# Performance work log

Measured on AMD Instinct MI355X. Metric: run time of the kernel, lower is better.

Reference implementation:

```python
import jax, jax.numpy as jnp
import numpy as np

ALPHA1 = 0.5
ALPHA2 = 0.5
EXP_WEIGHTED = False
N = 16384


def setup_inputs() -> dict:
    key = jax.random.key(0)
    k1, k2 = jax.random.split(key)
    inp = jax.random.normal(k1, (N,), dtype=jnp.float32)
    tgt = jax.random.uniform(k2, (N,), dtype=jnp.float32)
    return {"input": inp, "target": tgt}


def reference(input, target):
    n = input.shape[0]
    # mask[i, j] = target[j] > target[i]  (pairs where j is ranked above i)
    mask = target[None, :] > target[:, None]  # [N, N] bool
    # BPR term: log(1 + exp(-(input[j] - input[i]))) == softplus(input[i] - input[j])
    bpr = jax.nn.softplus(input[:, None] - input[None, :])  # [N, N]
    # MSE term depends only on row i, broadcast over j
    mse = (input - target) ** 2  # [N]
    x = ALPHA1 * bpr + ALPHA2 * mse[:, None]  # [N, N]
    if EXP_WEIGHTED:
        w = jnp.expm1(target)  # exp(target) - 1
        x = w[:, None] * w[None, :] * x
    # x[x < 0] = 0, and only masked pairs contribute
    x = jnp.where(mask, jnp.maximum(x, 0.0), 0.0)
    total = jnp.sum(x)
    if EXP_WEIGHTED:
        scale = 2.0 / (n * (jnp.e - 1.0)) ** 2
    else:
        scale = 2.0 / n ** 2
    return scale * total
```

## Files before the change

### kernel.cpp

```cpp
#include <hip/hip_runtime.h>


#define N_ELEM 16384
#define NBUCK  4096
#define CHUNK  256
#define NPAIR  511
#define NBLK   512
#define PF     0xAAAAAAAAu

__device__ __forceinline__ float fexp2(float x){ return __builtin_amdgcn_exp2f(x); }
__device__ __forceinline__ float flog2(float x){ return __builtin_amdgcn_logf(x); }

__global__ __launch_bounds__(1024, 8) void fused_kernel(
    const float* __restrict__ input, const float* __restrict__ target,
    float* __restrict__ wsA, int* __restrict__ cntA, int* __restrict__ gdone,
    float* __restrict__ out)
{
    const float L2E   = 1.4426950408889634f;
    const float INVN2 = 1.0f / (16384.0f * 16384.0f);
    const int b = blockIdx.x, tid = threadIdx.x, lane = tid & 63;
    const int wu = __builtin_amdgcn_readfirstlane((int)(threadIdx.x >> 6));

    __shared__ int histLds[NBUCK];
    __shared__ __align__(16) float cLds[CHUNK];
    __shared__ float wsLds[16];
    __shared__ int   wtot[16];

    float vsum = 0.0f;

    if (b == NPAIR) {
        for (int q = tid; q < NBUCK; q += 1024) histLds[q] = 0;
        __syncthreads();
        int packed[16];
        #pragma unroll
        for (int q = 0; q < 16; ++q) {
            const int idx = (q << 10) + tid;
            const float t = target[idx];
            int bk = (int)(t * 4096.0f);
            bk = bk < 0 ? 0 : (bk > 4095 ? 4095 : bk);
            const int ticket = atomicAdd(&histLds[bk], 1);
            packed[q] = (bk << 15) | ticket;
        }
        __syncthreads();
        int v[4], le[4]; int s = 0;
        #pragma unroll
        for (int q = 0; q < 4; ++q) v[q] = histLds[4 * tid + q];
        #pragma unroll
        for (int q = 0; q < 4; ++q) { le[q] = s; s += v[q]; }
        int inc = s;
        #pragma unroll
        for (int d = 1; d < 64; d <<= 1) {
            int n = __shfl_up(inc, d, 64); if (lane >= d) inc += n;
        }
        if (lane == 63) wtot[wu] = inc;
        __syncthreads();
        int woff = 0;
        #pragma unroll
        for (int w = 0; w < 16; ++w) woff += (w < wu) ? wtot[w] : 0;
        const int texcl = woff + (inc - s);
        #pragma unroll
        for (int q = 0; q < 4; ++q) histLds[4 * tid + q] = texcl + le[q];
        __syncthreads();
        #pragma unroll
        for (int q = 0; q < 16; ++q) {
            const int idx = (q << 10) + tid;
            const int pos = histLds[packed[q] >> 15] + (packed[q] & 0x7FFF);
            const float x = input[idx], t = target[idx];
            const float d = x - t;
            vsum += (-x * (float)pos + d * d * (float)(16383 - pos)) * INVN2;
        }
    } else {
        const int ntb = (b < 475) ? 4 : 5;
        const int u0  = (b < 475) ? (b << 2) : (1900 + 5 * (b - 475));
        int cj = (int)((sqrtf(8.0f * (float)u0 + 1.0f) - 1.0f) * 0.5f);
        while ((cj + 1) * (cj + 2) / 2 <= u0) ++cj;
        while (cj * (cj + 1) / 2 > u0) --cj;
        int ci = u0 - cj * (cj + 1) / 2;

        float la0 = 0.0f, la1 = 0.0f;
        int   cnt = 0;
        int   cjCur = -1;
        for (int m = 0; m < ntb; ++m) {
            if (cj != cjCur) {
                __syncthreads();
                if (tid < CHUNK)
                    cLds[tid] = 0.5f * fexp2(input[cj * CHUNK + tid] * L2E);
                cjCur = cj;
                __syncthreads();
            }
            float Xh[4];
            #pragma unroll
            for (int k = 0; k < 4; ++k)
                Xh[k] = 0.5f * fexp2(input[ci * CHUNK + 64 * k + lane] * L2E);
            const float4* __restrict__ cp4 = (const float4*)(cLds + wu * 16);
            const float4 A = cp4[0], B = cp4[1], C = cp4[2], D = cp4[3];

            if (ci != cj) {
                #pragma unroll
                for (int k = 0; k < 4; ++k) {
                    const float X = Xh[k];
                    float p = (X + A.x) * (X + A.y);
                    p *= (X + A.z) * (X + A.w);
                    p *= (X + B.x) * (X + B.y);
                    p *= (X + B.z) * (X + B.w);
                    p *= (X + C.x) * (X + C.y);
                    p *= (X + C.z) * (X + C.w);
                    p *= (X + D.x) * (X + D.y);
                    p *= (X + D.z) * (X + D.w);
                    if (k & 1) la1 += flog2(p); else la0 += flog2(p);
                }
                cnt += 64;
            } else {
                const int jb = wu * 16;
                #pragma unroll
                for (int k = 0; k < 4; ++k) {
                    const float X = Xh[k];
                    const int rr = 64 * k + lane;
                    float p = 1.0f; int c = 0;
                    #define PRD(col, q) do { const bool ok = (jb + (q)) > rr;   \
                        p *= ok ? (X + (col)) : 1.0f; c += ok ? 1 : 0; } while (0)
                    PRD(A.x,0);  PRD(A.y,1);  PRD(A.z,2);  PRD(A.w,3);
                    PRD(B.x,4);  PRD(B.y,5);  PRD(B.z,6);  PRD(B.w,7);
                    PRD(C.x,8);  PRD(C.y,9);  PRD(C.z,10); PRD(C.w,11);
                    PRD(D.x,12); PRD(D.y,13); PRD(D.z,14); PRD(D.w,15);
                    #undef PRD
                    if (k & 1) la1 += flog2(p); else la0 += flog2(p);
                    cnt += c;
                }
            }
            if (ci == cj) { ++cj; ci = 0; } else { ++ci; }
        }
        vsum = (la0 + la1 + (float)cnt) * (0.6931471805599453f * INVN2);
    }

    #pragma unroll
    for (int off = 32; off; off >>= 1) vsum += __shfl_down(vsum, off, 64);
    if (lane == 0) wsLds[wu] = vsum;
    __syncthreads();

    if (wu == 0) {
        float s = (lane < 16) ? wsLds[lane] : 0.0f;
        #pragma unroll
        for (int off = 8; off; off >>= 1) s += __shfl_down(s, off, 64);
        int isFinal = 0;
        if (lane == 0) {
            const int g = b & 63;
            float* slot  = wsA  + 32 * g;
            int*   cslot = cntA + 32 * g;
            const float old = __hip_atomic_fetch_add(slot, s,
                __ATOMIC_RELAXED, __HIP_MEMORY_SCOPE_AGENT);
            asm volatile("s_waitcnt vmcnt(0)" :: "v"(old) : "memory");
            const unsigned tkt = (unsigned)__hip_atomic_fetch_add(cslot, 1,
                __ATOMIC_RELAXED, __HIP_MEMORY_SCOPE_AGENT) - PF;
            if (tkt == 7u) {
                asm volatile("s_waitcnt vmcnt(0)" ::: "memory");
                const unsigned gd = (unsigned)__hip_atomic_fetch_add(gdone, 1,
                    __ATOMIC_RELAXED, __HIP_MEMORY_SCOPE_AGENT) - PF;
                isFinal = (gd == 63u);
            }
        }
        isFinal = __shfl(isFinal, 0, 64);
        if (isFinal) {
            float v = __hip_atomic_fetch_add(wsA + 32 * lane, 0.0f,
                __ATOMIC_RELAXED, __HIP_MEMORY_SCOPE_AGENT);
            #pragma unroll
            for (int off = 32; off; off >>= 1) v += __shfl_down(v, off, 64);
            if (lane == 0)
                out[0] = v - 64.0f * __uint_as_float(PF);
        }
    }
}

extern "C" void kernel_launch(void* const* d_in, const int* in_sizes, int n_in,
                              void* d_out, int out_size, void* d_ws, size_t ws_size,
                              hipStream_t stream) {
    const float* input  = (const float*)d_in[0];
    const float* target = (const float*)d_in[1];
    float* out   = (float*)d_out;
    int*   wsi   = (int*)d_ws;
    int*   gdone = wsi + 8;
    float* wsA   = (float*)d_ws + 32768;
    int*   cntA  = wsi + 65536;

    fused_kernel<<<NBLK, 1024, 0, stream>>>(input, target, wsA, cntA, gdone, out);
}
```

Before: 73.04 us.

## Symmetrize diagonal tiles and halve grid with more tiles per block

Diagonal tiles now compute the full unmasked product over all 256x256 pairs and take half, using the symmetry softplus(a-b)+softplus(b-a) = (a-b) + 2*softplus(b-a). The linear half-term and a ln2/2 offset per element move into the histogram block's per-element term. This removes the per-element masking and select work in diagonal tiles. The grid shrinks from 512 to 256 blocks, each handling 8 or 9 tiles, and the exp scaling is folded into an fma. Fewer blocks lowers launch and reduction overhead but gives less parallelism and a longer serial histogram block relative to the others.

```diff
diff --git a/kernel.cpp b/kernel.cpp
--- a/kernel.cpp
+++ b/kernel.cpp
@@ -4,14 +4,14 @@
 #define N_ELEM 16384
 #define NBUCK  4096
 #define CHUNK  256
-#define NPAIR  511
-#define NBLK   512
+#define NPAIR  255
+#define NBLK   256
 #define PF     0xAAAAAAAAu
 
 __device__ __forceinline__ float fexp2(float x){ return __builtin_amdgcn_exp2f(x); }
 __device__ __forceinline__ float flog2(float x){ return __builtin_amdgcn_logf(x); }
 
-__global__ __launch_bounds__(1024, 8) void fused_kernel(
+__global__ __launch_bounds__(1024) void fused_kernel(
     const float* __restrict__ input, const float* __restrict__ target,
     float* __restrict__ wsA, int* __restrict__ cntA, int* __restrict__ gdone,
     float* __restrict__ out)
@@ -67,70 +67,66 @@
             const int pos = histLds[packed[q] >> 15] + (packed[q] & 0x7FFF);
             const float x = input[idx], t = target[idx];
             const float d = x - t;
-            vsum += (-x * (float)pos + d * d * (float)(16383 - pos)) * INVN2;
+            vsum += (-x * ((float)pos + 0.5f)
+                     + d * d * (float)(16383 - pos)
+                     - 0.34657359027997264f) * INVN2;
         }
     } else {
-        const int ntb = (b < 475) ? 4 : 5;
-        const int u0  = (b < 475) ? (b << 2) : (1900 + 5 * (b - 475));
+        const int ntb = (b < 215) ? 8 : 9;
+        const int u0  = (b < 215) ? (b << 3) : (1720 + 9 * (b - 215));
         int cj = (int)((sqrtf(8.0f * (float)u0 + 1.0f) - 1.0f) * 0.5f);
         while ((cj + 1) * (cj + 2) / 2 <= u0) ++cj;
         while (cj * (cj + 1) / 2 > u0) --cj;
         int ci = u0 - cj * (cj + 1) / 2;
 
         float la0 = 0.0f, la1 = 0.0f;
-        int   cnt = 0;
+        float laD = 0.0f;
+        int   ntD = 0;
         int   cjCur = -1;
         for (int m = 0; m < ntb; ++m) {
             if (cj != cjCur) {
                 __syncthreads();
                 if (tid < CHUNK)
-                    cLds[tid] = 0.5f * fexp2(input[cj * CHUNK + tid] * L2E);
+                    cLds[tid] = fexp2(fmaf(input[cj * CHUNK + tid], L2E, -1.0f));
                 cjCur = cj;
                 __syncthreads();
             }
             float Xh[4];
             #pragma unroll
             for (int k = 0; k < 4; ++k)
-                Xh[k] = 0.5f * fexp2(input[ci * CHUNK + 64 * k + lane] * L2E);
+                Xh[k] = fexp2(fmaf(input[ci * CHUNK + 64 * k + lane], L2E, -1.0f));
             const float4* __restrict__ cp4 = (const float4*)(cLds + wu * 16);
             const float4 A = cp4[0], B = cp4[1], C = cp4[2], D = cp4[3];
 
+            float lg[4];
+            #pragma unroll
+            for (int k = 0; k < 4; ++k) {
+                const float X = Xh[k];
+                const float t0 = (X + A.x) * (X + A.y);
+                const float t1 = (X + A.z) * (X + A.w);
+                const float t2 = (X + B.x) * (X + B.y);
+                const float t3 = (X + B.z) * (X + B.w);
+                const float t4 = (X + C.x) * (X + C.y);
+                const float t5 = (X + C.z) * (X + C.w);
+                const float t6 = (X + D.x) * (X + D.y);
+                const float t7 = (X + D.z) * (X + D.w);
+                const float q0 = t0 * t1, q1 = t2 * t3;
+                const float q2 = t4 * t5, q3 = t6 * t7;
+                lg[k] = flog2((q0 * q1) * (q2 * q3));
+            }
             if (ci != cj) {
-                #pragma unroll
-                for (int k = 0; k < 4; ++k) {
-                    const float X = Xh[k];
-                    float p = (X + A.x) * (X + A.y);
-                    p *= (X + A.z) * (X + A.w);
-                    p *= (X + B.x) * (X + B.y);
-                    p *= (X + B.z) * (X + B.w);
-                    p *= (X + C.x) * (X + C.y);
-                    p *= (X + C.z) * (X + C.w);
-                    p *= (X + D.x) * (X + D.y);
-                    p *= (X + D.z) * (X + D.w);
-                    if (k & 1) la1 += flog2(p); else la0 += flog2(p);
-                }
-                cnt += 64;
+                la0 += lg[0] + lg[2];
+                la1 += lg[1] + lg[3];
             } else {
-                const int jb = wu * 16;
-                #pragma unroll
-                for (int k = 0; k < 4; ++k) {
-                    const float X = Xh[k];
-                    const int rr = 64 * k + lane;
-                    float p = 1.0f; int c = 0;
-                    #define PRD(col, q) do { const bool ok = (jb + (q)) > rr;   \
-                        p *= ok ? (X + (col)) : 1.0f; c += ok ? 1 : 0; } while (0)
-                    PRD(A.x,0);  PRD(A.y,1);  PRD(A.z,2);  PRD(A.w,3);
-                    PRD(B.x,4);  PRD(B.y,5);  PRD(B.z,6);  PRD(B.w,7);
-                    PRD(C.x,8);  PRD(C.y,9);  PRD(C.z,10); PRD(C.w,11);
-                    PRD(D.x,12); PRD(D.y,13); PRD(D.z,14); PRD(D.w,15);
-                    #undef PRD
-                    if (k & 1) la1 += flog2(p); else la0 += flog2(p);
-                    cnt += c;
-                }
+                laD += (lg[0] + lg[1]) + (lg[2] + lg[3]);
+                ++ntD;
             }
             if (ci == cj) { ++cj; ci = 0; } else { ++ci; }
         }
-        vsum = (la0 + la1 + (float)cnt) * (0.6931471805599453f * INVN2);
+        const float ntOff = (float)(ntb - ntD);
+        vsum = (la0 + la1 + 0.5f * laD
+                + 64.0f * (ntOff + 0.5f * (float)ntD))
+               * (0.6931471805599453f * INVN2);
     }
 
     #pragma unroll
@@ -152,7 +148,7 @@
             asm volatile("s_waitcnt vmcnt(0)" :: "v"(old) : "memory");
             const unsigned tkt = (unsigned)__hip_atomic_fetch_add(cslot, 1,
                 __ATOMIC_RELAXED, __HIP_MEMORY_SCOPE_AGENT) - PF;
-            if (tkt == 7u) {
+            if (tkt == 3u) {
                 asm volatile("s_waitcnt vmcnt(0)" ::: "memory");
                 const unsigned gd = (unsigned)__hip_atomic_fetch_add(gdone, 1,
                     __ATOMIC_RELAXED, __HIP_MEMORY_SCOPE_AGENT) - PF;
```

Result: faster. 66.81 us (-8.5%).
